# Kernel tuning notes

Hardware: AMD Instinct MI355X
Metric: run time of the kernel (lower is better)

The kernel has to match this reference:

```python
import jax, jax.numpy as jnp
import numpy as np

NUM_HEADS = 32
NUM_KV_HEADS = 8
HEAD_DIM = 128
ROPE_THETA = 10000.0
MAX_SEQ_LEN = 2048


def build_rope_cache(seq_len, head_dim, theta=10000.0):
    freq_indices = jnp.arange(0, head_dim, 2, dtype=jnp.float32)
    inv_freq = 1.0 / theta ** (freq_indices / head_dim)
    positions = jnp.arange(seq_len, dtype=jnp.float32)
    angles = jnp.outer(positions, inv_freq)  # (S, D/2)
    cos = jnp.cos(angles)
    sin = jnp.sin(angles)
    return jnp.concatenate([cos, cos], axis=-1), jnp.concatenate([sin, sin], axis=-1)


def apply_rotary_embedding(x, cos, sin):
    # x: (B, S, H, D); cos/sin: (S, D)
    d = x.shape[-1]
    x1, x2 = x[..., : d // 2], x[..., d // 2 :]
    x_rot = jnp.concatenate([-x2, x1], axis=-1)
    return x * cos[None, :, None, :] + x_rot * sin[None, :, None, :]


def setup_inputs() -> dict:
    key = jax.random.key(0)
    k_x, k_q, k_k, k_v, k_o = jax.random.split(key, 5)
    B, S, HID = 2, 2048, NUM_HEADS * HEAD_DIM
    KV = NUM_KV_HEADS * HEAD_DIM
    x = jax.random.normal(k_x, (B, S, HID), dtype=jnp.float32)
    # causal mask, shape (B, 1, S, S)
    causal = jnp.tril(jnp.ones((S, S), dtype=bool))
    mask = jnp.broadcast_to(causal[None, None], (B, 1, S, S))
    sc_in = 1.0 / np.sqrt(HID)
    Wq = jax.random.normal(k_q, (HID, HID), dtype=jnp.float32) * sc_in
    Wk = jax.random.normal(k_k, (HID, KV), dtype=jnp.float32) * sc_in
    Wv = jax.random.normal(k_v, (HID, KV), dtype=jnp.float32) * sc_in
    Wo = jax.random.normal(k_o, (HID, HID), dtype=jnp.float32) * sc_in
    return {"x": x, "mask": mask, "Wq": Wq, "Wk": Wk, "Wv": Wv, "Wo": Wo}


def reference(x, mask, Wq, Wk, Wv, Wo):
    B, S, _ = x.shape
    q = (x @ Wq).reshape(B, S, NUM_HEADS, HEAD_DIM)
    k = (x @ Wk).reshape(B, S, NUM_KV_HEADS, HEAD_DIM)
    v = (x @ Wv).reshape(B, S, NUM_KV_HEADS, HEAD_DIM)
    cos, sin = build_rope_cache(MAX_SEQ_LEN, HEAD_DIM, ROPE_THETA)
    cos, sin = cos[:S], sin[:S]
    q = apply_rotary_embedding(q, cos, sin)
    k = apply_rotary_embedding(k, cos, sin)
    group = NUM_HEADS // NUM_KV_HEADS
    if group > 1:
        k = jnp.repeat(k, group, axis=2)
        v = jnp.repeat(v, group, axis=2)
    scale = HEAD_DIM ** -0.5
    # (B, H, S, S)
    scores = jnp.einsum("bqhd,bkhd->bhqk", q, k) * scale
    scores = jnp.where(mask, scores, jnp.finfo(jnp.float32).min)
    attn = jax.nn.softmax(scores, axis=-1)
    out = jnp.einsum("bhqk,bkhd->bqhd", attn, v).reshape(B, S, NUM_HEADS * HEAD_DIM)
    return out @ Wo
```

## Files before the change

kernel.cpp:

```cpp
#include <hip/hip_runtime.h>

#define S_LEN   2048
#define HID_DIM 4096
#define NHEADS  32
#define NKVH    8
#define HD      128
#define KV_DIM  1024
#define KV2     2048
#define BS_ROWS 4096

typedef __attribute__((ext_vector_type(4))) float f32x4;
typedef __attribute__((ext_vector_type(8))) short bf16x8;

__device__ __forceinline__ unsigned short f2b(float f) {
  union { float f; unsigned int u; } cv; cv.f = f;
  unsigned int r = (cv.u + 0x7FFFu + ((cv.u >> 16) & 1u)) >> 16;
  return (unsigned short)r;
}
__device__ __forceinline__ float b2f(unsigned short u) {
  union { unsigned int u; float f; } cv; cv.u = ((unsigned int)u) << 16; return cv.f;
}
__device__ __forceinline__ void gload_lds16(const void* g, void* l) {
  __builtin_amdgcn_global_load_lds(
      (const __attribute__((address_space(1))) unsigned int*)g,
      (__attribute__((address_space(3))) unsigned int*)l, 16, 0, 0);
}
__device__ __forceinline__ void store_out(float* p, float v) { *p = v; }
__device__ __forceinline__ void store_out(unsigned short* p, float v) { *p = f2b(v); }

__global__ void cvt_f32_bf16(const float* __restrict__ in, unsigned short* __restrict__ out, int n4) {
  int i = blockIdx.x * blockDim.x + threadIdx.x;
  if (i >= n4) return;
  f32x4 v = reinterpret_cast<const f32x4*>(in)[i];
  ushort4 o;
  o.x = f2b(v[0]); o.y = f2b(v[1]); o.z = f2b(v[2]); o.w = f2b(v[3]);
  reinterpret_cast<ushort4*>(out)[i] = o;
}

__global__ void transpose_cvt(const float* __restrict__ W, unsigned short* __restrict__ Wt,
                              int K, int N) {
  __shared__ float t[32][33];
  int n0 = blockIdx.x * 32, k0 = blockIdx.y * 32;
  int tx = threadIdx.x, ty = threadIdx.y;
#pragma unroll
  for (int i = 0; i < 4; ++i)
    t[ty + 8 * i][tx] = W[(size_t)(k0 + ty + 8 * i) * N + n0 + tx];
  __syncthreads();
#pragma unroll
  for (int i = 0; i < 4; ++i)
    Wt[(size_t)(n0 + ty + 8 * i) * K + k0 + tx] = f2b(t[tx][ty + 8 * i]);
}

__global__ void transpose_v_k(const unsigned short* __restrict__ KVb, unsigned short* __restrict__ Vt) {
  __shared__ unsigned short t[32][33];
  int c0 = blockIdx.x * 32;
  int r0 = blockIdx.y * 32;
  int tx = threadIdx.x, ty = threadIdx.y;
#pragma unroll
  for (int i = 0; i < 4; ++i)
    t[ty + 8 * i][tx] = KVb[(size_t)(r0 + ty + 8 * i) * KV2 + KV_DIM + c0 + tx];
  __syncthreads();
  int ob = (r0 >> 11) * 1024;
  int oc = r0 & 2047;
#pragma unroll
  for (int i = 0; i < 4; ++i)
    Vt[(size_t)(ob + c0 + ty + 8 * i) * S_LEN + oc + tx] = t[tx][ty + 8 * i];
}

__global__ void rope_table_k(float* __restrict__ cosT, float* __restrict__ sinT) {
  int idx = blockIdx.x * blockDim.x + threadIdx.x;
  if (idx >= S_LEN * 64) return;
  int s = idx >> 6, i = idx & 63;
  float inv = 1.0f / powf(10000.0f, (float)(2 * i) * (1.0f / 128.0f));
  float ang = (float)s * inv;
  cosT[idx] = cosf(ang);
  sinT[idx] = sinf(ang);
}

__global__ void rope_apply_k(unsigned short* __restrict__ X, const float* __restrict__ cosT,
                             const float* __restrict__ sinT, int nheads, int rowstride,
                             float scale, int total) {
  int idx = blockIdx.x * blockDim.x + threadIdx.x;
  if (idx >= total) return;
  int i4 = idx & 15;
  int t = idx >> 4;
  int h = t % nheads;
  int row = t / nheads;
  int s = row & (S_LEN - 1);
  f32x4 c4 = *reinterpret_cast<const f32x4*>(&cosT[(s << 6) + i4 * 4]);
  f32x4 s4 = *reinterpret_cast<const f32x4*>(&sinT[(s << 6) + i4 * 4]);
  size_t base = (size_t)row * rowstride + (size_t)h * HD + i4 * 4;
  ushort4 xa = *reinterpret_cast<const ushort4*>(&X[base]);
  ushort4 xb = *reinterpret_cast<const ushort4*>(&X[base + 64]);
  unsigned short* pa = (unsigned short*)&xa;
  unsigned short* pb = (unsigned short*)&xb;
  ushort4 oa, ob;
  unsigned short* qa = (unsigned short*)&oa;
  unsigned short* qb = (unsigned short*)&ob;
#pragma unroll
  for (int j = 0; j < 4; ++j) {
    float x1 = b2f(pa[j]), x2 = b2f(pb[j]);
    qa[j] = f2b((x1 * c4[j] - x2 * s4[j]) * scale);
    qb[j] = f2b((x2 * c4[j] + x1 * s4[j]) * scale);
  }
  *reinterpret_cast<ushort4*>(&X[base])      = oa;
  *reinterpret_cast<ushort4*>(&X[base + 64]) = ob;
}

template <typename OutT>
__global__ __launch_bounds__(256) void gemm_bt(const unsigned short* __restrict__ A,
                                               const unsigned short* __restrict__ Bt,
                                               OutT* __restrict__ C, int M, int N, int K) {
  __shared__ unsigned short As[128 * 32];
  __shared__ unsigned short Bs[128 * 32];
  const int tid = threadIdx.x;
  const int lane = tid & 63;
  const int wave = tid >> 6;
  int nwg = gridDim.x, wg = blockIdx.x;
  int swz = (nwg % 8 == 0) ? ((wg & 7) * (nwg >> 3) + (wg >> 3)) : wg;
  const int nbn = N >> 7;
  const int bm = swz / nbn, bn = swz % nbn;
  const int m0 = bm << 7, n0 = bn << 7;
  const int wr = wave >> 1, wc = wave & 1;
  const int lr = lane & 15, kb = lane >> 4;

  f32x4 acc[4][4];
#pragma unroll
  for (int i = 0; i < 4; ++i)
#pragma unroll
    for (int j = 0; j < 4; ++j) acc[i][j] = (f32x4){0.f, 0.f, 0.f, 0.f};

  const unsigned short* Ab = A + (size_t)m0 * K;
  const unsigned short* Bb = Bt + (size_t)n0 * K;

  for (int k0 = 0; k0 < K; k0 += 32) {
    __syncthreads();
#pragma unroll
    for (int i = 0; i < 2; ++i) {
      int idx = i * 256 + tid;
      int row = idx >> 2;
      int off = (idx & 3) << 3;
      gload_lds16(Ab + (size_t)row * K + k0 + off, As + row * 32 + off);
      gload_lds16(Bb + (size_t)row * K + k0 + off, Bs + row * 32 + off);
    }
    __syncthreads();

    bf16x8 af[4], bfr[4];
#pragma unroll
    for (int mi = 0; mi < 4; ++mi)
      af[mi] = *reinterpret_cast<const bf16x8*>(As + (wr * 64 + mi * 16 + lr) * 32 + kb * 8);
#pragma unroll
    for (int ni = 0; ni < 4; ++ni)
      bfr[ni] = *reinterpret_cast<const bf16x8*>(Bs + (wc * 64 + ni * 16 + lr) * 32 + kb * 8);
#pragma unroll
    for (int mi = 0; mi < 4; ++mi)
#pragma unroll
      for (int ni = 0; ni < 4; ++ni)
        acc[mi][ni] = __builtin_amdgcn_mfma_f32_16x16x32_bf16(af[mi], bfr[ni], acc[mi][ni], 0, 0, 0);
  }

#pragma unroll
  for (int mi = 0; mi < 4; ++mi)
#pragma unroll
    for (int ni = 0; ni < 4; ++ni)
#pragma unroll
      for (int r = 0; r < 4; ++r) {
        int row = m0 + wr * 64 + mi * 16 + kb * 4 + r;
        int col = n0 + wc * 64 + ni * 16 + lr;
        store_out(&C[(size_t)row * N + col], acc[mi][ni][r]);
      }
}

#define STAGE_HALF(dstBase, Sp, k0, h)                                           \
  {                                                                              \
    _Pragma("unroll")                                                            \
    for (int i_ = 0; i_ < 2; ++i_) {                                             \
      int c_ = i_ * 512 + tid;                                                   \
      int rl_ = c_ >> 3, ch_ = c_ & 7;                                           \
      int row_ = (h) * 128 + rl_;                                                \
      gload_lds16((Sp) + (size_t)row_ * K + (k0) + ((ch_ ^ (row_ & 7)) << 3),    \
                  (char*)(dstBase) + row_ * 128 + ch_ * 16);                     \
    }                                                                            \
  }
#define LDF(buf, R, sw) \
  (*reinterpret_cast<const bf16x8*>((const char*)(buf) + (R) * 128 + (sw)))
#define PHASE_SYNC()                                        \
  __builtin_amdgcn_s_barrier();                             \
  asm volatile("s_waitcnt lgkmcnt(0)" ::: "memory");        \
  __builtin_amdgcn_sched_barrier(0);

template <typename OutT>
__global__ __launch_bounds__(512, 1) void gemm256(const unsigned short* __restrict__ A,
                                                  const unsigned short* __restrict__ Bt,
                                                  OutT* __restrict__ C, int M, int N, int K) {
  __shared__ unsigned short Asl[2][256 * 64];
  __shared__ unsigned short Bsl[2][256 * 64];
  const int tid = threadIdx.x;
  const int lane = tid & 63;
  const int wave = tid >> 6;
  const int wr = wave >> 2;
  const int wc = wave & 3;
  const int lr = lane & 15, kb = lane >> 4;

  int nwg = gridDim.x, wg = blockIdx.x;
  int swz = (nwg % 8 == 0) ? ((wg & 7) * (nwg >> 3) + (wg >> 3)) : wg;
  const int nbn = N >> 8;
  const int bm = swz / nbn, bn = swz % nbn;
  const int m0 = bm << 8, n0 = bn << 8;

  const unsigned short* Ab = A + (size_t)m0 * K;
  const unsigned short* Bb = Bt + (size_t)n0 * K;

  f32x4 acc[8][4];
#pragma unroll
  for (int i = 0; i < 8; ++i)
#pragma unroll
    for (int j = 0; j < 4; ++j) acc[i][j] = (f32x4){0.f, 0.f, 0.f, 0.f};

  const int sw0 = ((kb) ^ (lr & 7)) << 4;
  const int sw1 = ((4 + kb) ^ (lr & 7)) << 4;

  STAGE_HALF(Asl[0], Ab, 0, 0); STAGE_HALF(Asl[0], Ab, 0, 1);
  STAGE_HALF(Bsl[0], Bb, 0, 0); STAGE_HALF(Bsl[0], Bb, 0, 1);
  __syncthreads();

  const int nt = K >> 6;
  bf16x8 af[4], bfr[4];

#pragma unroll 1
  for (int t = 0; t < nt; ++t) {
    const unsigned short* Acur = Asl[t & 1];
    const unsigned short* Bcur = Bsl[t & 1];
    unsigned short* Anxt = Asl[(t + 1) & 1];
    unsigned short* Bnxt = Bsl[(t + 1) & 1];
    const int k0n = (t + 1) << 6;
    const bool pf = (t + 1 < nt);

#pragma unroll
    for (int ni = 0; ni < 4; ++ni) bfr[ni] = LDF(Bcur, wc * 64 + ni * 16 + lr, sw0);
#pragma unroll
    for (int mi = 0; mi < 4; ++mi) af[mi] = LDF(Acur, wr * 128 + mi * 16 + lr, sw0);
    if (pf) { STAGE_HALF(Anxt, Ab, k0n, 0); STAGE_HALF(Anxt, Ab, k0n, 1); }
    PHASE_SYNC();
    __builtin_amdgcn_s_setprio(1);
#pragma unroll
    for (int mi = 0; mi < 4; ++mi)
#pragma unroll
      for (int ni = 0; ni < 4; ++ni)
        acc[mi][ni] = __builtin_amdgcn_mfma_f32_16x16x32_bf16(af[mi], bfr[ni], acc[mi][ni], 0, 0, 0);
    __builtin_amdgcn_s_setprio(0);
    __builtin_amdgcn_s_barrier();

#pragma unroll
    for (int mi = 0; mi < 4; ++mi) af[mi] = LDF(Acur, wr * 128 + (mi + 4) * 16 + lr, sw0);
    if (pf) { STAGE_HALF(Bnxt, Bb, k0n, 0); STAGE_HALF(Bnxt, Bb, k0n, 1); }
    PHASE_SYNC();
    __builtin_amdgcn_s_setprio(1);
#pragma unroll
    for (int mi = 0; mi < 4; ++mi)
#pragma unroll
      for (int ni = 0; ni < 4; ++ni)
        acc[mi + 4][ni] = __builtin_amdgcn_mfma_f32_16x16x32_bf16(af[mi], bfr[ni], acc[mi + 4][ni], 0, 0, 0);
    __builtin_amdgcn_s_setprio(0);
    __builtin_amdgcn_s_barrier();

#pragma unroll
    for (int ni = 0; ni < 4; ++ni) bfr[ni] = LDF(Bcur, wc * 64 + ni * 16 + lr, sw1);
#pragma unroll
    for (int mi = 0; mi < 4; ++mi) af[mi] = LDF(Acur, wr * 128 + mi * 16 + lr, sw1);
    PHASE_SYNC();
    __builtin_amdgcn_s_setprio(1);
#pragma unroll
    for (int mi = 0; mi < 4; ++mi)
#pragma unroll
      for (int ni = 0; ni < 4; ++ni)
        acc[mi][ni] = __builtin_amdgcn_mfma_f32_16x16x32_bf16(af[mi], bfr[ni], acc[mi][ni], 0, 0, 0);
    __builtin_amdgcn_s_setprio(0);
    __builtin_amdgcn_s_barrier();

#pragma unroll
    for (int mi = 0; mi < 4; ++mi) af[mi] = LDF(Acur, wr * 128 + (mi + 4) * 16 + lr, sw1);
    PHASE_SYNC();
    __builtin_amdgcn_s_setprio(1);
#pragma unroll
    for (int mi = 0; mi < 4; ++mi)
#pragma unroll
      for (int ni = 0; ni < 4; ++ni)
        acc[mi + 4][ni] = __builtin_amdgcn_mfma_f32_16x16x32_bf16(af[mi], bfr[ni], acc[mi + 4][ni], 0, 0, 0);
    __builtin_amdgcn_s_setprio(0);
    __builtin_amdgcn_s_barrier();

    if (pf) asm volatile("s_waitcnt vmcnt(0)" ::: "memory");
    __builtin_amdgcn_s_barrier();
  }

#pragma unroll
  for (int mi = 0; mi < 8; ++mi)
#pragma unroll
    for (int ni = 0; ni < 4; ++ni)
#pragma unroll
      for (int r = 0; r < 4; ++r) {
        int row = m0 + wr * 128 + mi * 16 + kb * 4 + r;
        int col = n0 + wc * 64 + ni * 16 + lr;
        store_out(&C[(size_t)row * N + col], acc[mi][ni][r]);
      }
}

__global__ __launch_bounds__(256) void attn_fwd(const unsigned short* __restrict__ Q,
                                                const unsigned short* __restrict__ KV,
                                                const unsigned short* __restrict__ Vt,
                                                const float* __restrict__ cosT,
                                                const float* __restrict__ sinT,
                                                unsigned short* __restrict__ O) {
  __shared__ unsigned short Ks[2][64 * 128];
  __shared__ unsigned short Ps[4][16 * 72];
  const int tid = threadIdx.x, lane = tid & 63, wave = tid >> 6;
  const int lr = lane & 15, kb = lane >> 4;
  const int pr = blockIdx.x;
  const int bh = blockIdx.y;
  const int b = bh >> 5, h = bh & 31, kvh = h >> 2;
  const unsigned short* Qp = Q + (size_t)b * S_LEN * HID_DIM + (size_t)h * HD;
  const unsigned short* Kp = KV + (size_t)b * S_LEN * KV2 + (size_t)kvh * HD;
  const unsigned short* Vtp = Vt + (size_t)(b * 8 + kvh) * HD * S_LEN;
  unsigned short* Op = O + (size_t)b * S_LEN * HID_DIM + (size_t)h * HD;

#pragma unroll 1
  for (int pass = 0; pass < 2; ++pass) {
    const int qt = pass ? pr : 31 - pr;
    const int q0 = qt * 64;
    const int qrow = q0 + wave * 16 + lr;

    bf16x8 qf[4];
    {
      bf16x8 raw[4];
#pragma unroll
      for (int dc = 0; dc < 4; ++dc)
        raw[dc] = *reinterpret_cast<const bf16x8*>(Qp + (size_t)qrow * HID_DIM + dc * 32 + kb * 8);
      const float* ct = cosT + (qrow << 6) + kb * 8;
      const float* st = sinT + (qrow << 6) + kb * 8;
      f32x4 cv0 = *(const f32x4*)(ct),      cv1 = *(const f32x4*)(ct + 4);
      f32x4 cv2 = *(const f32x4*)(ct + 32), cv3 = *(const f32x4*)(ct + 36);
      f32x4 sv0 = *(const f32x4*)(st),      sv1 = *(const f32x4*)(st + 4);
      f32x4 sv2 = *(const f32x4*)(st + 32), sv3 = *(const f32x4*)(st + 36);
      const float sc = 0.08838834764831843f;
#pragma unroll
      for (int j = 0; j < 8; ++j) {
        const int jj = j & 3;
        float c0 = (j < 4) ? cv0[jj] : cv1[jj];
        float s0 = (j < 4) ? sv0[jj] : sv1[jj];
        float c1 = (j < 4) ? cv2[jj] : cv3[jj];
        float s1 = (j < 4) ? sv2[jj] : sv3[jj];
        float a1 = b2f((unsigned short)raw[0][j]), a2 = b2f((unsigned short)raw[2][j]);
        qf[0][j] = (short)f2b((a1 * c0 - a2 * s0) * sc);
        qf[2][j] = (short)f2b((a2 * c0 + a1 * s0) * sc);
        float b1 = b2f((unsigned short)raw[1][j]), b2x = b2f((unsigned short)raw[3][j]);
        qf[1][j] = (short)f2b((b1 * c1 - b2x * s1) * sc);
        qf[3][j] = (short)f2b((b2x * c1 + b1 * s1) * sc);
      }
    }

    f32x4 of[8];
#pragma unroll
    for (int i = 0; i < 8; ++i) of[i] = (f32x4){0.f, 0.f, 0.f, 0.f};
    float mrow = -3.0e38f, lrow = 0.f;

    const int nsteps = qt + 1;

#pragma unroll
    for (int i = 0; i < 4; ++i) {
      int c = i * 256 + tid;
      int key = c >> 4;
      int ch = (c & 15) ^ (key & 7);
      gload_lds16(Kp + (size_t)key * KV2 + ch * 8, &Ks[0][0] + c * 8);
    }
    __syncthreads();

#pragma unroll 1
    for (int t = 0; t < nsteps; ++t) {
      const int kv0 = t << 6;
      const unsigned short* Kcur = &Ks[t & 1][0];

      bf16x8 vf[8];
#pragma unroll
      for (int dc2 = 0; dc2 < 8; ++dc2)
        vf[dc2] = *reinterpret_cast<const bf16x8*>(
            Vtp + (size_t)(dc2 * 16 + lr) * S_LEN + kv0 + kb * 8);

      if (t + 1 < nsteps) {
        unsigned short* Knxt = &Ks[(t + 1) & 1][0];
#pragma unroll
        for (int i = 0; i < 4; ++i) {
          int c = i * 256 + tid;
          int key = c >> 4;
          int ch = (c & 15) ^ (key & 7);
          gload_lds16(Kp + (size_t)(kv0 + 64 + key) * KV2 + ch * 8, Knxt + c * 8);
        }
      }

      f32x4 sf[4];
#pragma unroll
      for (int ki = 0; ki < 4; ++ki) {
        sf[ki] = (f32x4){0.f, 0.f, 0.f, 0.f};
#pragma unroll
        for (int dc = 0; dc < 4; ++dc) {
          bf16x8 kf = *reinterpret_cast<const bf16x8*>(
              Kcur + (ki * 16 + lr) * 128 + (((dc * 4 + kb) ^ (lr & 7)) << 3));
          sf[ki] = __builtin_amdgcn_mfma_f32_16x16x32_bf16(kf, qf[dc], sf[ki], 0, 0, 0);
        }
      }

      if (kv0 + 63 > q0 + wave * 16) {
        const int thr = qrow - kv0;
#pragma unroll
        for (int ki = 0; ki < 4; ++ki)
#pragma unroll
          for (int r = 0; r < 4; ++r)
            if (ki * 16 + kb * 4 + r > thr) sf[ki][r] = -3.0e38f;
      }

      float m8 = -3.0e38f;
#pragma unroll
      for (int ki = 0; ki < 4; ++ki)
#pragma unroll
        for (int r = 0; r < 4; ++r) m8 = fmaxf(m8, sf[ki][r]);
      m8 = fmaxf(m8, __shfl_xor(m8, 16));
      m8 = fmaxf(m8, __shfl_xor(m8, 32));
      if (__any(m8 > mrow + 8.0f)) {
        float mn = fmaxf(mrow, m8);
        float corr = __expf(mrow - mn);
        lrow *= corr;
#pragma unroll
        for (int r = 0; r < 4; ++r) {
          float cr = __shfl(corr, kb * 4 + r);
#pragma unroll
          for (int dc2 = 0; dc2 < 8; ++dc2) of[dc2][r] *= cr;
        }
        mrow = mn;
      }
      float rs = 0.f;
      ushort4 pw[4];
#pragma unroll
      for (int ki = 0; ki < 4; ++ki) {
        unsigned short* pp = (unsigned short*)&pw[ki];
#pragma unroll
        for (int r = 0; r < 4; ++r) {
          float p = __expf(sf[ki][r] - mrow);
          rs += p;
          pp[r] = f2b(p);
        }
      }
      rs += __shfl_xor(rs, 16);
      rs += __shfl_xor(rs, 32);
      lrow += rs;

#pragma unroll
      for (int ki = 0; ki < 4; ++ki)
        *reinterpret_cast<ushort4*>(&Ps[wave][lr * 72 + ki * 16 + kb * 4]) = pw[ki];
      asm volatile("s_waitcnt lgkmcnt(0)" ::: "memory");
      __builtin_amdgcn_sched_barrier(0);

      bf16x8 pf = *reinterpret_cast<const bf16x8*>(&Ps[wave][lr * 72 + kb * 8]);
#pragma unroll
      for (int dc2 = 0; dc2 < 8; ++dc2)
        of[dc2] = __builtin_amdgcn_mfma_f32_16x16x32_bf16(pf, vf[dc2], of[dc2], 0, 0, 0);

#pragma unroll
      for (int dc2 = 0; dc2 < 8; ++dc2)
        vf[dc2] = *reinterpret_cast<const bf16x8*>(
            Vtp + (size_t)(dc2 * 16 + lr) * S_LEN + kv0 + 32 + kb * 8);
      pf = *reinterpret_cast<const bf16x8*>(&Ps[wave][lr * 72 + 32 + kb * 8]);
#pragma unroll
      for (int dc2 = 0; dc2 < 8; ++dc2)
        of[dc2] = __builtin_amdgcn_mfma_f32_16x16x32_bf16(pf, vf[dc2], of[dc2], 0, 0, 0);

      __syncthreads();
    }

    float linv[4];
#pragma unroll
    for (int r = 0; r < 4; ++r) linv[r] = 1.0f / __shfl(lrow, kb * 4 + r);
#pragma unroll
    for (int dc2 = 0; dc2 < 8; ++dc2)
#pragma unroll
      for (int r = 0; r < 4; ++r) {
        int qg = q0 + wave * 16 + kb * 4 + r;
        Op[(size_t)qg * HID_DIM + dc2 * 16 + lr] = f2b(of[dc2][r] * linv[r]);
      }
  }
}

extern "C" void kernel_launch(void* const* d_in, const int* in_sizes, int n_in,
                              void* d_out, int out_size, void* d_ws, size_t ws_size,
                              hipStream_t stream) {
  const float* x  = (const float*)d_in[0];
  const float* Wq = (const float*)d_in[2];
  const float* Wk = (const float*)d_in[3];
  const float* Wv = (const float*)d_in[4];
  const float* Wo = (const float*)d_in[5];
  float* out = (float*)d_out;

  char* ws = (char*)d_ws;
  unsigned short* xb  = (unsigned short*)(ws + 0);
  unsigned short* wtb = (unsigned short*)(ws + 33554432);
  unsigned short* wkt = (unsigned short*)(ws + 67108864);
  unsigned short* wvt = (unsigned short*)(ws + 75497472);
  unsigned short* Qb  = (unsigned short*)(ws + 83886080);
  unsigned short* KVb = (unsigned short*)(ws + 117440512);
  float* cosT = (float*)(ws + 134217728);
  float* sinT = (float*)(ws + 134742016);
  unsigned short* AO  = xb;
  unsigned short* Vtb = wkt;

  cvt_f32_bf16<<<16384, 256, 0, stream>>>(x, xb, (BS_ROWS * HID_DIM) / 4);
  transpose_cvt<<<dim3(128, 128), dim3(32, 8), 0, stream>>>(Wq, wtb, HID_DIM, HID_DIM);
  transpose_cvt<<<dim3(32, 128), dim3(32, 8), 0, stream>>>(Wk, wkt, HID_DIM, KV_DIM);
  transpose_cvt<<<dim3(32, 128), dim3(32, 8), 0, stream>>>(Wv, wvt, HID_DIM, KV_DIM);
  rope_table_k<<<512, 256, 0, stream>>>(cosT, sinT);

  gemm256<unsigned short><<<256, 512, 0, stream>>>(xb, wtb, Qb, BS_ROWS, HID_DIM, HID_DIM);
  gemm_bt<unsigned short><<<512, 256, 0, stream>>>(xb, wkt, KVb, BS_ROWS, KV2, HID_DIM);

  transpose_v_k<<<dim3(32, 128), dim3(32, 8), 0, stream>>>(KVb, Vtb);
  transpose_cvt<<<dim3(128, 128), dim3(32, 8), 0, stream>>>(Wo, wtb, HID_DIM, HID_DIM);

  rope_apply_k<<<2048, 256, 0, stream>>>(KVb, cosT, sinT, NKVH, KV2, 1.0f,
                                         BS_ROWS * NKVH * 16);

  attn_fwd<<<dim3(16, 64), 256, 0, stream>>>(Qb, KVb, Vtb, cosT, sinT, AO);

  gemm256<float><<<256, 512, 0, stream>>>(AO, wtb, out, BS_ROWS, HID_DIM, HID_DIM);
}
```

Before: 670.9 us.

## Process 128-row query tiles per block, with two query sub-tiles per wave

The attention kernel now handles 128 query rows per block, each wave owning two 16-row query sub-tiles, so every K tile in LDS and every V fragment loaded from global memory is reused across twice as many queries. K is no longer double-buffered and is loaded synchronously each step behind two barriers. Launch bounds add a minimum of 2 blocks per CU and the grid halves. Risks are higher register pressure from the doubled accumulators, fewer blocks for load balance, and lost overlap of the K load with compute.

Result: faster. 583.0 us (-13.1%).

```diff
diff --git a/kernel.cpp b/kernel.cpp
--- a/kernel.cpp
+++ b/kernel.cpp
@@ -306,14 +306,14 @@
       }
 }
 
-__global__ __launch_bounds__(256) void attn_fwd(const unsigned short* __restrict__ Q,
-                                                const unsigned short* __restrict__ KV,
-                                                const unsigned short* __restrict__ Vt,
-                                                const float* __restrict__ cosT,
-                                                const float* __restrict__ sinT,
-                                                unsigned short* __restrict__ O) {
-  __shared__ unsigned short Ks[2][64 * 128];
-  __shared__ unsigned short Ps[4][16 * 72];
+__global__ __launch_bounds__(256, 2) void attn_fwd(const unsigned short* __restrict__ Q,
+                                                   const unsigned short* __restrict__ KV,
+                                                   const unsigned short* __restrict__ Vt,
+                                                   const float* __restrict__ cosT,
+                                                   const float* __restrict__ sinT,
+                                                   unsigned short* __restrict__ O) {
+  __shared__ unsigned short Ks[64 * 128];
+  __shared__ unsigned short Ps[4][2][16 * 72];
   const int tid = threadIdx.x, lane = tid & 63, wave = tid >> 6;
   const int lr = lane & 15, kb = lane >> 4;
   const int pr = blockIdx.x;
@@ -326,12 +326,16 @@
 
 #pragma unroll 1
   for (int pass = 0; pass < 2; ++pass) {
-    const int qt = pass ? pr : 31 - pr;
-    const int q0 = qt * 64;
-    const int qrow = q0 + wave * 16 + lr;
-
-    bf16x8 qf[4];
-    {
+    const int qt = pass ? pr : 15 - pr;
+    const int q0 = qt * 128;
+    int qrowQ[2];
+    qrowQ[0] = q0 + wave * 32 + lr;
+    qrowQ[1] = q0 + wave * 32 + 16 + lr;
+
+    bf16x8 qf[2][4];
+#pragma unroll
+    for (int qs = 0; qs < 2; ++qs) {
+      const int qrow = qrowQ[qs];
       bf16x8 raw[4];
 #pragma unroll
       for (int dc = 0; dc < 4; ++dc)
@@ -351,141 +355,149 @@
         float c1 = (j < 4) ? cv2[jj] : cv3[jj];
         float s1 = (j < 4) ? sv2[jj] : sv3[jj];
         float a1 = b2f((unsigned short)raw[0][j]), a2 = b2f((unsigned short)raw[2][j]);
-        qf[0][j] = (short)f2b((a1 * c0 - a2 * s0) * sc);
-        qf[2][j] = (short)f2b((a2 * c0 + a1 * s0) * sc);
+        qf[qs][0][j] = (short)f2b((a1 * c0 - a2 * s0) * sc);
+        qf[qs][2][j] = (short)f2b((a2 * c0 + a1 * s0) * sc);
         float b1 = b2f((unsigned short)raw[1][j]), b2x = b2f((unsigned short)raw[3][j]);
-        qf[1][j] = (short)f2b((b1 * c1 - b2x * s1) * sc);
-        qf[3][j] = (short)f2b((b2x * c1 + b1 * s1) * sc);
+        qf[qs][1][j] = (short)f2b((b1 * c1 - b2x * s1) * sc);
+        qf[qs][3][j] = (short)f2b((b2x * c1 + b1 * s1) * sc);
       }
     }
 
-    f32x4 of[8];
-#pragma unroll
-    for (int i = 0; i < 8; ++i) of[i] = (f32x4){0.f, 0.f, 0.f, 0.f};
-    float mrow = -3.0e38f, lrow = 0.f;
-
-    const int nsteps = qt + 1;
-
-#pragma unroll
-    for (int i = 0; i < 4; ++i) {
-      int c = i * 256 + tid;
-      int key = c >> 4;
-      int ch = (c & 15) ^ (key & 7);
-      gload_lds16(Kp + (size_t)key * KV2 + ch * 8, &Ks[0][0] + c * 8);
-    }
-    __syncthreads();
+    f32x4 of[2][8];
+#pragma unroll
+    for (int qs = 0; qs < 2; ++qs)
+#pragma unroll
+      for (int i = 0; i < 8; ++i) of[qs][i] = (f32x4){0.f, 0.f, 0.f, 0.f};
+    float mrow[2] = {-3.0e38f, -3.0e38f};
+    float lrow[2] = {0.f, 0.f};
+
+    const int nsteps = 2 * qt + 2;
 
 #pragma unroll 1
     for (int t = 0; t < nsteps; ++t) {
       const int kv0 = t << 6;
-      const unsigned short* Kcur = &Ks[t & 1][0];
-
+      __syncthreads();
+#pragma unroll
+      for (int i = 0; i < 4; ++i) {
+        int c = i * 256 + tid;
+        int key = c >> 4;
+        int ch = (c & 15) ^ (key & 7);
+        gload_lds16(Kp + (size_t)(kv0 + key) * KV2 + ch * 8, Ks + c * 8);
+      }
       bf16x8 vf[8];
 #pragma unroll
       for (int dc2 = 0; dc2 < 8; ++dc2)
         vf[dc2] = *reinterpret_cast<const bf16x8*>(
             Vtp + (size_t)(dc2 * 16 + lr) * S_LEN + kv0 + kb * 8);
-
-      if (t + 1 < nsteps) {
-        unsigned short* Knxt = &Ks[(t + 1) & 1][0];
-#pragma unroll
-        for (int i = 0; i < 4; ++i) {
-          int c = i * 256 + tid;
-          int key = c >> 4;
-          int ch = (c & 15) ^ (key & 7);
-          gload_lds16(Kp + (size_t)(kv0 + 64 + key) * KV2 + ch * 8, Knxt + c * 8);
-        }
-      }
-
-      f32x4 sf[4];
-#pragma unroll
-      for (int ki = 0; ki < 4; ++ki) {
-        sf[ki] = (f32x4){0.f, 0.f, 0.f, 0.f};
+      __syncthreads();
+
+      f32x4 sf[2][4];
+#pragma unroll
+      for (int qs = 0; qs < 2; ++qs)
+#pragma unroll
+        for (int ki = 0; ki < 4; ++ki) sf[qs][ki] = (f32x4){0.f, 0.f, 0.f, 0.f};
+#pragma unroll
+      for (int ki = 0; ki < 4; ++ki)
 #pragma unroll
         for (int dc = 0; dc < 4; ++dc) {
           bf16x8 kf = *reinterpret_cast<const bf16x8*>(
-              Kcur + (ki * 16 + lr) * 128 + (((dc * 4 + kb) ^ (lr & 7)) << 3));
-          sf[ki] = __builtin_amdgcn_mfma_f32_16x16x32_bf16(kf, qf[dc], sf[ki], 0, 0, 0);
-        }
-      }
-
-      if (kv0 + 63 > q0 + wave * 16) {
-        const int thr = qrow - kv0;
+              Ks + (ki * 16 + lr) * 128 + (((dc * 4 + kb) ^ (lr & 7)) << 3));
+          sf[0][ki] = __builtin_amdgcn_mfma_f32_16x16x32_bf16(kf, qf[0][dc], sf[0][ki], 0, 0, 0);
+          sf[1][ki] = __builtin_amdgcn_mfma_f32_16x16x32_bf16(kf, qf[1][dc], sf[1][ki], 0, 0, 0);
+        }
+
+#pragma unroll
+      for (int qs = 0; qs < 2; ++qs) {
+        if (kv0 + 63 > q0 + wave * 32 + qs * 16) {
+          const int thr = qrowQ[qs] - kv0;
+#pragma unroll
+          for (int ki = 0; ki < 4; ++ki)
+#pragma unroll
+            for (int r = 0; r < 4; ++r)
+              if (ki * 16 + kb * 4 + r > thr) sf[qs][ki][r] = -3.0e38f;
+        }
+      }
+
+#pragma unroll
+      for (int qs = 0; qs < 2; ++qs) {
+        float m8 = -3.0e38f;
 #pragma unroll
         for (int ki = 0; ki < 4; ++ki)
 #pragma unroll
-          for (int r = 0; r < 4; ++r)
-            if (ki * 16 + kb * 4 + r > thr) sf[ki][r] = -3.0e38f;
-      }
-
-      float m8 = -3.0e38f;
-#pragma unroll
-      for (int ki = 0; ki < 4; ++ki)
-#pragma unroll
-        for (int r = 0; r < 4; ++r) m8 = fmaxf(m8, sf[ki][r]);
-      m8 = fmaxf(m8, __shfl_xor(m8, 16));
-      m8 = fmaxf(m8, __shfl_xor(m8, 32));
-      if (__any(m8 > mrow + 8.0f)) {
-        float mn = fmaxf(mrow, m8);
-        float corr = __expf(mrow - mn);
-        lrow *= corr;
-#pragma unroll
-        for (int r = 0; r < 4; ++r) {
-          float cr = __shfl(corr, kb * 4 + r);
-#pragma unroll
-          for (int dc2 = 0; dc2 < 8; ++dc2) of[dc2][r] *= cr;
-        }
-        mrow = mn;
-      }
-      float rs = 0.f;
-      ushort4 pw[4];
-#pragma unroll
-      for (int ki = 0; ki < 4; ++ki) {
-        unsigned short* pp = (unsigned short*)&pw[ki];
-#pragma unroll
-        for (int r = 0; r < 4; ++r) {
-          float p = __expf(sf[ki][r] - mrow);
-          rs += p;
-          pp[r] = f2b(p);
-        }
-      }
-      rs += __shfl_xor(rs, 16);
-      rs += __shfl_xor(rs, 32);
-      lrow += rs;
-
-#pragma unroll
-      for (int ki = 0; ki < 4; ++ki)
-        *reinterpret_cast<ushort4*>(&Ps[wave][lr * 72 + ki * 16 + kb * 4]) = pw[ki];
+          for (int r = 0; r < 4; ++r) m8 = fmaxf(m8, sf[qs][ki][r]);
+        m8 = fmaxf(m8, __shfl_xor(m8, 16));
+        m8 = fmaxf(m8, __shfl_xor(m8, 32));
+        if (__any(m8 > mrow[qs] + 8.0f)) {
+          float mn = fmaxf(mrow[qs], m8);
+          float corr = __expf(mrow[qs] - mn);
+          lrow[qs] *= corr;
+#pragma unroll
+          for (int r = 0; r < 4; ++r) {
+            float cr = __shfl(corr, kb * 4 + r);
+#pragma unroll
+            for (int dc2 = 0; dc2 < 8; ++dc2) of[qs][dc2][r] *= cr;
+          }
+          mrow[qs] = mn;
+        }
+        float rs = 0.f;
+        ushort4 pw[4];
+#pragma unroll
+        for (int ki = 0; ki < 4; ++ki) {
+          unsigned short* pp = (unsigned short*)&pw[ki];
+#pragma unroll
+          for (int r = 0; r < 4; ++r) {
+            float p = __expf(sf[qs][ki][r] - mrow[qs]);
+            rs += p;
+            pp[r] = f2b(p);
+          }
+        }
+        rs += __shfl_xor(rs, 16);
+        rs += __shfl_xor(rs, 32);
+        lrow[qs] += rs;
+#pragma unroll
+        for (int ki = 0; ki < 4; ++ki)
+          *reinterpret_cast<ushort4*>(&Ps[wave][qs][lr * 72 + ki * 16 + kb * 4]) = pw[ki];
+      }
       asm volatile("s_waitcnt lgkmcnt(0)" ::: "memory");
       __builtin_amdgcn_sched_barrier(0);
 
-      bf16x8 pf = *reinterpret_cast<const bf16x8*>(&Ps[wave][lr * 72 + kb * 8]);
-#pragma unroll
-      for (int dc2 = 0; dc2 < 8; ++dc2)
-        of[dc2] = __builtin_amdgcn_mfma_f32_16x16x32_bf16(pf, vf[dc2], of[dc2], 0, 0, 0);
-
+      {
+        bf16x8 pf0 = *reinterpret_cast<const bf16x8*>(&Ps[wave][0][lr * 72 + kb * 8]);
+        bf16x8 pf1 = *reinterpret_cast<const bf16x8*>(&Ps[wave][1][lr * 72 + kb * 8]);
+#pragma unroll
+        for (int dc2 = 0; dc2 < 8; ++dc2) {
+          of[0][dc2] = __builtin_amdgcn_mfma_f32_16x16x32_bf16(pf0, vf[dc2], of[0][dc2], 0, 0, 0);
+          of[1][dc2] = __builtin_amdgcn_mfma_f32_16x16x32_bf16(pf1, vf[dc2], of[1][dc2], 0, 0, 0);
+        }
+      }
 #pragma unroll
       for (int dc2 = 0; dc2 < 8; ++dc2)
         vf[dc2] = *reinterpret_cast<const bf16x8*>(
             Vtp + (size_t)(dc2 * 16 + lr) * S_LEN + kv0 + 32 + kb * 8);
-      pf = *reinterpret_cast<const bf16x8*>(&Ps[wave][lr * 72 + 32 + kb * 8]);
+      {
+        bf16x8 pf0 = *reinterpret_cast<const bf16x8*>(&Ps[wave][0][lr * 72 + 32 + kb * 8]);
+        bf16x8 pf1 = *reinterpret_cast<const bf16x8*>(&Ps[wave][1][lr * 72 + 32 + kb * 8]);
+#pragma unroll
+        for (int dc2 = 0; dc2 < 8; ++dc2) {
+          of[0][dc2] = __builtin_amdgcn_mfma_f32_16x16x32_bf16(pf0, vf[dc2], of[0][dc2], 0, 0, 0);
+          of[1][dc2] = __builtin_amdgcn_mfma_f32_16x16x32_bf16(pf1, vf[dc2], of[1][dc2], 0, 0, 0);
+        }
+      }
+    }
+
+#pragma unroll
+    for (int qs = 0; qs < 2; ++qs) {
+      float linv[4];
+#pragma unroll
+      for (int r = 0; r < 4; ++r) linv[r] = 1.0f / __shfl(lrow[qs], kb * 4 + r);
 #pragma unroll
       for (int dc2 = 0; dc2 < 8; ++dc2)
-        of[dc2] = __builtin_amdgcn_mfma_f32_16x16x32_bf16(pf, vf[dc2], of[dc2], 0, 0, 0);
-
-      __syncthreads();
+#pragma unroll
+        for (int r = 0; r < 4; ++r) {
+          int qg = q0 + wave * 32 + qs * 16 + kb * 4 + r;
+          Op[(size_t)qg * HID_DIM + dc2 * 16 + lr] = f2b(of[qs][dc2][r] * linv[r]);
+        }
     }
-
-    float linv[4];
-#pragma unroll
-    for (int r = 0; r < 4; ++r) linv[r] = 1.0f / __shfl(lrow, kb * 4 + r);
-#pragma unroll
-    for (int dc2 = 0; dc2 < 8; ++dc2)
-#pragma unroll
-      for (int r = 0; r < 4; ++r) {
-        int qg = q0 + wave * 16 + kb * 4 + r;
-        Op[(size_t)qg * HID_DIM + dc2 * 16 + lr] = f2b(of[dc2][r] * linv[r]);
-      }
   }
 }
 
@@ -526,7 +538,7 @@
   rope_apply_k<<<2048, 256, 0, stream>>>(KVb, cosT, sinT, NKVH, KV2, 1.0f,
                                          BS_ROWS * NKVH * 16);
 
-  attn_fwd<<<dim3(16, 64), 256, 0, stream>>>(Qb, KVb, Vtb, cosT, sinT, AO);
+  attn_fwd<<<dim3(8, 64), 256, 0, stream>>>(Qb, KVb, Vtb, cosT, sinT, AO);
 
   gemm256<float><<<256, 512, 0, stream>>>(AO, wtb, out, BS_ROWS, HID_DIM, HID_DIM);
 }
```
